# Kernel optimization log

Hardware: AMD Instinct MI355X
Metric: run time of the kernel (lower is better)

The kernel has to match this reference:

```python
import jax, jax.numpy as jnp
import numpy as np

B, S, D, V, H, L, NM = 16, 512, 768, 30522, 12, 12, 77
HD = D // H  # 64
FF = 4 * D
EPS = 1e-5


def setup_inputs() -> dict:
    key = jax.random.key(0)
    ks = jax.random.split(key, 32)
    sc = 0.02
    n = lambda k, shp: jax.random.normal(k, shp, dtype=jnp.float32) * sc
    d = {}
    d["token_ids"] = jax.random.randint(ks[0], (B, S), 0, V)
    d["segment_ids"] = jax.random.randint(ks[1], (B, S), 0, 2)
    d["mask_ids"] = jax.random.randint(ks[2], (B, NM), 0, S)
    d["tok_emb"] = n(ks[3], (V, D))
    d["pos_emb"] = n(ks[4], (S, D))
    d["seg_emb"] = n(ks[5], (2, D))
    d["dense_w"] = n(ks[6], (V, D))
    d["dense_b"] = jnp.zeros((V,), jnp.float32)
    # per-layer params stacked on leading L axis (torch Linear convention: y = x @ W.T + b)
    d["Wq"] = n(ks[7], (L, D, D)); d["bq"] = jnp.zeros((L, D), jnp.float32)
    d["Wk"] = n(ks[8], (L, D, D)); d["bk"] = jnp.zeros((L, D), jnp.float32)
    d["Wv"] = n(ks[9], (L, D, D)); d["bv"] = jnp.zeros((L, D), jnp.float32)
    d["Wo"] = n(ks[10], (L, D, D)); d["bo"] = jnp.zeros((L, D), jnp.float32)
    d["W1"] = n(ks[11], (L, FF, D)); d["b1"] = jnp.zeros((L, FF), jnp.float32)
    d["W2"] = n(ks[12], (L, D, FF)); d["b2"] = jnp.zeros((L, D), jnp.float32)
    d["g1"] = jnp.ones((L, D), jnp.float32); d["be1"] = jnp.zeros((L, D), jnp.float32)
    d["g2"] = jnp.ones((L, D), jnp.float32); d["be2"] = jnp.zeros((L, D), jnp.float32)
    return d


def _ln(x, g, b):
    m = jnp.mean(x, -1, keepdims=True)
    v = jnp.mean(jnp.square(x - m), -1, keepdims=True)
    return (x - m) * jax.lax.rsqrt(v + EPS) * g + b


def _encoder_stack(x, layer_params):
    def layer(x, p):
        Wq, bq, Wk, bk, Wv, bv, Wo, bo, W1, b1, W2, b2, g1, be1, g2, be2 = p
        q = (x @ Wq.T + bq).reshape(B, S, H, HD).transpose(0, 2, 1, 3)  # bhsd
        k = (x @ Wk.T + bk).reshape(B, S, H, HD).transpose(0, 2, 1, 3)
        v = (x @ Wv.T + bv).reshape(B, S, H, HD).transpose(0, 2, 1, 3)
        scores = jnp.einsum('bhqd,bhkd->bhqk', q, k) / jnp.sqrt(jnp.float32(HD))
        attn = jax.nn.softmax(scores, axis=-1)
        o = jnp.einsum('bhqk,bhkd->bhqd', attn, v).transpose(0, 2, 1, 3).reshape(B, S, D)
        x = _ln(x + (o @ Wo.T + bo), g1, be1)
        h = jax.nn.gelu(x @ W1.T + b1, approximate=False)  # torch nn.GELU default is exact
        h = h @ W2.T + b2
        return _ln(x + h, g2, be2), None
    x, _ = jax.lax.scan(layer, x, layer_params)
    return x


def reference(token_ids, segment_ids, mask_ids, tok_emb, pos_emb, seg_emb,
              dense_w, dense_b, Wq, bq, Wk, bk, Wv, bv, Wo, bo,
              W1, b1, W2, b2, g1, be1, g2, be2):
    x = tok_emb[token_ids] + seg_emb[segment_ids] + pos_emb[None, :, :]  # [B,S,D]
    x = _encoder_stack(x, (Wq, bq, Wk, bk, Wv, bv, Wo, bo, W1, b1, W2, b2, g1, be1, g2, be2))
    idx = jnp.broadcast_to(mask_ids[:, :, None], (B, NM, D))
    out = jnp.take_along_axis(x, idx, axis=1)  # [B,NM,D]
    return out @ dense_w.T + dense_b  # [B,NM,V]
```

## Files before the change

kernel.cpp:

```cpp
#include <hip/hip_runtime.h>
#include <stdint.h>

typedef uint16_t u16;
typedef uint32_t u32;
typedef uint64_t u64;
typedef short short8 __attribute__((ext_vector_type(8)));
typedef float f32x4 __attribute__((ext_vector_type(4)));

#define DEV static __device__ __forceinline__

DEV u16 f2bf(float f){
  u32 x = __builtin_bit_cast(u32, f);
  return (u16)((x + 0x7fffu + ((x >> 16) & 1u)) >> 16);
}

DEV float bf2f(u16 u){
  u32 v = (u32)u << 16;
  return __builtin_bit_cast(float, v);
}

DEV f32x4 mfma16(short8 a, short8 b, f32x4 c){
  return __builtin_amdgcn_mfma_f32_16x16x32_bf16(a, b, c, 0, 0, 0);
}

DEV void async16(const void* g, void* l){
  __builtin_amdgcn_global_load_lds(
      (const __attribute__((address_space(1))) u32*)g,
      (__attribute__((address_space(3))) u32*)l, 16, 0, 0);
}

__global__ __launch_bounds__(256)
void embed_kernel(const int* __restrict__ tid, const int* __restrict__ sid,
                  const float* __restrict__ tok, const float* __restrict__ pos,
                  const float* __restrict__ seg, u16* __restrict__ xb)
{
  const int row = blockIdx.x;
  const int s = row & 511;
  const int tk = tid[row], sg = sid[row];
  const int t = threadIdx.x;
#pragma unroll
  for (int e = 0; e < 3; ++e){
    int i = t + e*256;
    float v = tok[(u64)tk*768 + i] + seg[(u64)sg*768 + i] + pos[(u64)s*768 + i];
    xb[(u64)row*768 + i] = f2bf(v);
  }
}

__global__ __launch_bounds__(256)
void cvt_bf16(const float4* __restrict__ in, ushort4* __restrict__ out, int n4)
{
  int i = blockIdx.x*256 + threadIdx.x;
  if (i >= n4) return;
  float4 f = in[i];
  ushort4 o;
  o.x = f2bf(f.x); o.y = f2bf(f.y); o.z = f2bf(f.z); o.w = f2bf(f.w);
  out[i] = o;
}

__global__ __launch_bounds__(256)
void cvt_layer(const float4* __restrict__ Wq, const float4* __restrict__ Wk,
               const float4* __restrict__ Wv, const float4* __restrict__ Wo,
               const float4* __restrict__ W1, const float4* __restrict__ W2,
               ushort4* __restrict__ wqkv, ushort4* __restrict__ wob,
               ushort4* __restrict__ w1b, ushort4* __restrict__ w2b)
{
  const int i = blockIdx.x*256 + threadIdx.x;
  const int S = 147456;
  float4 f; ushort4* dst; int di;
  if      (i <   S)       { f = Wq[i];            dst = wqkv; di = i; }
  else if (i < 2*S)       { f = Wk[i - S];        dst = wqkv; di = i; }
  else if (i < 3*S)       { f = Wv[i - 2*S];      dst = wqkv; di = i; }
  else if (i < 4*S)       { f = Wo[i - 3*S];      dst = wob;  di = i - 3*S; }
  else if (i < 4*S+589824){ f = W1[i - 4*S];      dst = w1b;  di = i - 4*S; }
  else                    { f = W2[i - 4*S-589824]; dst = w2b; di = i - 4*S - 589824; }
  ushort4 o;
  o.x = f2bf(f.x); o.y = f2bf(f.y); o.z = f2bf(f.z); o.w = f2bf(f.w);
  dst[di] = o;
}

__global__ __launch_bounds__(256)
void concat_bias(const float* __restrict__ bq, const float* __restrict__ bk,
                 const float* __restrict__ bv, float* __restrict__ out)
{
  const int l = blockIdx.x;
  const int t = threadIdx.x;
#pragma unroll
  for (int e = 0; e < 3; ++e){
    int i = t + e*256;
    out[(u64)l*2304 + i]        = bq[(u64)l*768 + i];
    out[(u64)l*2304 + 768 + i]  = bk[(u64)l*768 + i];
    out[(u64)l*2304 + 1536 + i] = bv[(u64)l*768 + i];
  }
}

DEV void stage128(const u16* __restrict__ X, int ld, int limit,
                  int rowbase, int k0, u16* lds, int t)
{
  const int rl  = t >> 2;
  const int col = (((t & 3) ^ ((t >> 3) & 3))) << 3;
  int r0 = rowbase + rl;       if (r0 > limit-1) r0 = limit-1;
  int r1 = rowbase + rl + 64;  if (r1 > limit-1) r1 = limit-1;
  async16(X + (u64)r0*ld + k0 + col, lds + t*8);
  async16(X + (u64)r1*ld + k0 + col, lds + 2048 + t*8);
}

DEV short8 ldfrag(const u16* buf, int row, int slot){
  return *(const short8*)(buf + row*32 + (slot << 3));
}

template<int EPI>
__global__ __launch_bounds__(256)
void gemm3r(const u16* __restrict__ A, const u16* __restrict__ W,
            const float* __restrict__ bias, const u16* __restrict__ xres,
            u16* __restrict__ vt, void* __restrict__ Cout,
            int M, int N, int K, int GM)
{
  __shared__ u16 sm[24576];
  const int t = threadIdx.x;
  const int w = t >> 6, l = t & 63;
  const int lr = l & 15, lg = l >> 4;
  const int wm = (w >> 1)*64, wn = (w & 1)*64;
  const int xr = (lr >> 1) & 3;
  const int slot = lg ^ xr;

  const int nwg = gridDim.x, orig = blockIdx.x;
  const int q = nwg >> 3, r = nwg & 7;
  const int xcd = orig & 7, sl8 = orig >> 3;
  const int wgid = (xcd < r ? xcd*(q+1) : r*(q+1) + (xcd-r)*q) + sl8;
  const int bm = wgid % GM, bn = wgid / GM;

  f32x4 acc[4][4] = {};
  short8 af[4], bf[4];

  const int NT = K >> 5;
  stage128(A, K, M, bm*128,  0, sm,          t);
  stage128(W, K, N, bn*128,  0, sm + 4096,   t);
  stage128(A, K, M, bm*128, 32, sm + 8192,   t);
  stage128(W, K, N, bn*128, 32, sm + 12288,  t);
  asm volatile("s_waitcnt vmcnt(4)" ::: "memory");
  __builtin_amdgcn_s_barrier();

  for (int tt = 0; tt < NT; ++tt){
    const int rs  = (tt % 3) * 8192;
    const int rs2 = ((tt + 2) % 3) * 8192;
    const int k2  = (tt + 2) * 32;
    const bool st2 = (tt + 2) < NT;
    const u16* Ar = sm + rs;
    const u16* Br = sm + rs + 4096;

    af[0] = ldfrag(Ar, wm + lr, slot);
    af[1] = ldfrag(Ar, wm + 16 + lr, slot);
#pragma unroll
    for (int ni = 0; ni < 4; ++ni) bf[ni] = ldfrag(Br, wn + ni*16 + lr, slot);
    if (st2) stage128(A, K, M, bm*128, k2, sm + rs2, t);
    __builtin_amdgcn_s_barrier();
    __builtin_amdgcn_s_setprio(1);
#pragma unroll
    for (int mi = 0; mi < 2; ++mi)
#pragma unroll
      for (int ni = 0; ni < 4; ++ni)
        acc[mi][ni] = mfma16(af[mi], bf[ni], acc[mi][ni]);
    __builtin_amdgcn_s_setprio(0);
    __builtin_amdgcn_s_barrier();

    af[2] = ldfrag(Ar, wm + 32 + lr, slot);
    af[3] = ldfrag(Ar, wm + 48 + lr, slot);
    if (st2) stage128(W, K, N, bn*128, k2, sm + rs2 + 4096, t);
    __builtin_amdgcn_s_barrier();
    __builtin_amdgcn_s_setprio(1);
#pragma unroll
    for (int mi = 2; mi < 4; ++mi)
#pragma unroll
      for (int ni = 0; ni < 4; ++ni)
        acc[mi][ni] = mfma16(af[mi], bf[ni], acc[mi][ni]);
    __builtin_amdgcn_s_setprio(0);
    if (st2) asm volatile("s_waitcnt vmcnt(4)" ::: "memory");
    else     asm volatile("s_waitcnt vmcnt(0)" ::: "memory");
    __builtin_amdgcn_s_barrier();
  }

  __syncthreads();

  if constexpr (EPI == 1){
    if (vt && bn*128 + wn >= 1536){
      u16* vbuf = sm + w*4736;
#pragma unroll
      for (int mi = 0; mi < 4; ++mi)
#pragma unroll
        for (int ni = 0; ni < 4; ++ni){
          int col = bn*128 + wn + ni*16 + lr;
          float bv = bias ? bias[col] : 0.f;
#pragma unroll
          for (int rr = 0; rr < 4; ++rr)
            vbuf[(mi*16 + lg*4 + rr)*74 + ni*16 + lr] = f2bf(acc[mi][ni][rr] + bv);
        }
      asm volatile("s_waitcnt lgkmcnt(0)" ::: "memory");
      const int row0w = bm*128 + wm;
      const int b_ = row0w >> 9, s0 = row0w & 511;
      const int h_ = (bn*128 + wn - 1536) >> 6;
#pragma unroll
      for (int e = 0; e < 8; ++e){
        int d = e*8 + (l >> 3), s8 = (l & 7)*8;
        short8 ov;
#pragma unroll
        for (int i = 0; i < 8; ++i) ov[i] = (short)vbuf[(s8 + i)*74 + d];
        *(short8*)(vt + ((u64)(b_*12 + h_)*64 + d)*512 + s0 + s8) = ov;
      }
      return;
    }
  }

  constexpr int EPLD = 68;
  float* epw = (float*)sm + w*(16*EPLD);
#pragma unroll
  for (int mi = 0; mi < 4; ++mi){
#pragma unroll
    for (int ni = 0; ni < 4; ++ni){
      int col = bn*128 + wn + ni*16 + lr;
      float bv = bias ? bias[col < N ? col : N-1] : 0.f;
#pragma unroll
      for (int rr = 0; rr < 4; ++rr){
        float v = acc[mi][ni][rr] + bv;
        if constexpr (EPI == 2) v = 0.5f*v*(1.0f + erff(v*0.70710678118f));
        epw[(lg*4 + rr)*EPLD + ni*16 + lr] = v;
      }
    }
    asm volatile("s_waitcnt lgkmcnt(0)" ::: "memory");
    if constexpr (EPI == 0){
#pragma unroll
      for (int ps = 0; ps < 4; ++ps){
        int rloc = ps*4 + (l >> 4);
        int row = bm*128 + wm + mi*16 + rloc;
        int col = bn*128 + wn + (l & 15)*4;
        f32x4 v4 = *(const f32x4*)&epw[rloc*EPLD + (l & 15)*4];
        if (row < M){
          if (col + 3 < N){
            if (xres){
              ushort4 x4 = *(const ushort4*)(xres + (u64)row*N + col);
              v4[0] += bf2f(x4.x); v4[1] += bf2f(x4.y);
              v4[2] += bf2f(x4.z); v4[3] += bf2f(x4.w);
            }
            *(f32x4*)((float*)Cout + (u64)row*N + col) = v4;
          } else {
#pragma unroll
            for (int j = 0; j < 4; ++j)
              if (col + j < N){
                float vv = v4[j];
                if (xres) vv += bf2f(xres[(u64)row*N + col + j]);
                ((float*)Cout)[(u64)row*N + col + j] = vv;
              }
          }
        }
      }
    } else {
#pragma unroll
      for (int ps = 0; ps < 2; ++ps){
        int rloc = ps*8 + (l >> 3);
        int row = bm*128 + wm + mi*16 + rloc;
        int col = bn*128 + wn + (l & 7)*8;
        f32x4 a4 = *(const f32x4*)&epw[rloc*EPLD + (l & 7)*8];
        f32x4 b4 = *(const f32x4*)&epw[rloc*EPLD + (l & 7)*8 + 4];
        short8 o8;
        o8[0] = f2bf(a4[0]); o8[1] = f2bf(a4[1]); o8[2] = f2bf(a4[2]); o8[3] = f2bf(a4[3]);
        o8[4] = f2bf(b4[0]); o8[5] = f2bf(b4[1]); o8[6] = f2bf(b4[2]); o8[7] = f2bf(b4[3]);
        if (row < M){
          if (col + 7 < N) *(short8*)((u16*)Cout + (u64)row*N + col) = o8;
          else {
#pragma unroll
            for (int j = 0; j < 8; ++j)
              if (col + j < N) ((u16*)Cout)[(u64)row*N + col + j] = (u16)o8[j];
          }
        }
      }
    }
    asm volatile("s_waitcnt lgkmcnt(0)" ::: "memory");
  }
}

DEV void stage_tile(const u16* __restrict__ X, int ld, int limit,
                    int rowbase, int k0, u16* lds, int t)
{
  const int rl  = t >> 2;
  const int col = (((t & 3) ^ ((t >> 3) & 3))) << 3;
  int r0 = rowbase + rl;        if (r0 > limit-1) r0 = limit-1;
  int r1 = rowbase + rl + 128;  if (r1 > limit-1) r1 = limit-1;
  async16(X + (u64)r0*ld + k0 + col, lds + t*8);
  async16(X + (u64)r1*ld + k0 + col, lds + 4096 + t*8);
}

__global__ __launch_bounds__(512)
void gemm8v(const u16* __restrict__ A, const u16* __restrict__ W,
            const float* __restrict__ bias, float* __restrict__ Cout,
            int M, int N, int K, int GM)
{
  __shared__ u16 sm[49152];
  u16* Ab = sm;
  u16* Bb = sm + 24576;
  const int t = threadIdx.x;
  const int w = t >> 6, l = t & 63;
  const int lr = l & 15, lg = l >> 4;
  const int wr = w >> 2, wc = w & 3;
  const int xr = (lr >> 1) & 3;
  const int slot = lg ^ xr;

  const int nwg = gridDim.x, orig = blockIdx.x;
  const int q = nwg >> 3, r = nwg & 7;
  const int xcd = orig & 7, sl8 = orig >> 3;
  const int wgid = (xcd < r ? xcd*(q+1) : r*(q+1) + (xcd-r)*q) + sl8;
  const int bm = wgid % GM, bn = wgid / GM;

  f32x4 acc[8][4] = {};
  short8 afr[4], bfr[4];

  const int NT = K >> 5;
  stage_tile(A, K, M, bm*256,  0, Ab,        t);
  stage_tile(W, K, N, bn*256,  0, Bb,        t);
  stage_tile(A, K, M, bm*256, 32, Ab + 8192, t);
  stage_tile(W, K, N, bn*256, 32, Bb + 8192, t);
  asm volatile("s_waitcnt vmcnt(4)" ::: "memory");
  __builtin_amdgcn_s_barrier();

  for (int tt = 0; tt < NT; ++tt){
    const int rs = (tt % 3) * 8192;
    const int rs2 = ((tt + 2) % 3) * 8192;
    const int k2 = (tt + 2)*32;
    const u16* Ar = Ab + rs;
    const u16* Br = Bb + rs;
#pragma unroll
    for (int mi = 0; mi < 4; ++mi) afr[mi] = ldfrag(Ar, wr*128 + mi*16 + lr, slot);
#pragma unroll
    for (int ni = 0; ni < 4; ++ni) bfr[ni] = ldfrag(Br, wc*64 + ni*16 + lr, slot);
    if (tt + 2 < NT) stage_tile(A, K, M, bm*256, k2, Ab + rs2, t);
    __builtin_amdgcn_s_barrier();
    __builtin_amdgcn_s_setprio(1);
#pragma unroll
    for (int mi = 0; mi < 4; ++mi)
#pragma unroll
      for (int ni = 0; ni < 4; ++ni)
        acc[mi][ni] = mfma16(afr[mi], bfr[ni], acc[mi][ni]);
    __builtin_amdgcn_s_setprio(0);
    __builtin_amdgcn_s_barrier();
#pragma unroll
    for (int mi = 0; mi < 4; ++mi) afr[mi] = ldfrag(Ar, wr*128 + (mi+4)*16 + lr, slot);
    if (tt + 2 < NT) stage_tile(W, K, N, bn*256, k2, Bb + rs2, t);
    __builtin_amdgcn_s_barrier();
    __builtin_amdgcn_s_setprio(1);
#pragma unroll
    for (int mi = 0; mi < 4; ++mi)
#pragma unroll
      for (int ni = 0; ni < 4; ++ni)
        acc[mi+4][ni] = mfma16(afr[mi], bfr[ni], acc[mi+4][ni]);
    __builtin_amdgcn_s_setprio(0);
    if (tt + 2 < NT) asm volatile("s_waitcnt vmcnt(4)" ::: "memory");
    else             asm volatile("s_waitcnt vmcnt(0)" ::: "memory");
    __builtin_amdgcn_s_barrier();
  }

  __syncthreads();
  constexpr int EPLD = 68;
  float* epw = (float*)sm + w*(16*EPLD);
  const int growbase = bm*256 + wr*128;
  const int gcolbase = bn*256 + wc*64;
#pragma unroll
  for (int mi = 0; mi < 8; ++mi){
#pragma unroll
    for (int ni = 0; ni < 4; ++ni){
      int col = gcolbase + ni*16 + lr;
      float bv = bias ? bias[col < N ? col : N-1] : 0.f;
#pragma unroll
      for (int rr = 0; rr < 4; ++rr)
        epw[(lg*4 + rr)*EPLD + ni*16 + lr] = acc[mi][ni][rr] + bv;
    }
    asm volatile("s_waitcnt lgkmcnt(0)" ::: "memory");
#pragma unroll
    for (int ps = 0; ps < 4; ++ps){
      int rloc = ps*4 + (l >> 4);
      int row = growbase + mi*16 + rloc;
      int col = gcolbase + (l & 15)*4;
      f32x4 v4 = *(const f32x4*)&epw[rloc*EPLD + (l & 15)*4];
      if (row < M){
        if (col + 3 < N) *(f32x4*)(Cout + (u64)row*N + col) = v4;
        else {
#pragma unroll
          for (int j = 0; j < 4; ++j)
            if (col + j < N) Cout[(u64)row*N + col + j] = v4[j];
        }
      }
    }
    asm volatile("s_waitcnt lgkmcnt(0)" ::: "memory");
  }
}

__global__ __launch_bounds__(256)
void attn_kernel(const u16* __restrict__ qkv, const u16* __restrict__ vt,
                 u16* __restrict__ ob)
{
  __shared__ u16 p_lds[4][32][72];
  const int t = threadIdx.x, w = t >> 6, ll = t & 63;
  const int lr = ll & 15, lg = ll >> 4;
  const int qt = blockIdx.x, h = blockIdx.y, b = blockIdx.z;
  const int q0 = qt*128 + w*32;
  const float C = 0.125f * 1.44269504f;

  short8 qf[2][2];
#pragma unroll
  for (int f = 0; f < 2; ++f){
    const u16* qrow = qkv + (u64)(b*512 + q0 + f*16 + lr)*2304 + h*64 + 8*lg;
    qf[f][0] = *(const short8*)qrow;
    qf[f][1] = *(const short8*)(qrow + 32);
  }

  const u16* kbh = qkv + (u64)(b*512)*2304 + 768 + h*64;
  const u16* vth = vt + (u64)(b*12 + h)*64*512;

  f32x4 lacc[2] = {};
  f32x4 o_acc[2][4] = {};

  for (int jt = 0; jt < 8; ++jt){
    const int jb = jt*64;
    f32x4 s[2][4] = {};
#pragma unroll
    for (int jn = 0; jn < 4; ++jn){
      const u16* kr = kbh + (u64)(jb + jn*16 + lr)*2304 + 8*lg;
      short8 kf0 = *(const short8*)kr;
      short8 kf1 = *(const short8*)(kr + 32);
#pragma unroll
      for (int f = 0; f < 2; ++f){
        s[f][jn] = mfma16(qf[f][0], kf0, s[f][jn]);
        s[f][jn] = mfma16(qf[f][1], kf1, s[f][jn]);
      }
    }
#pragma unroll
    for (int f = 0; f < 2; ++f)
#pragma unroll
      for (int jn = 0; jn < 4; ++jn)
#pragma unroll
        for (int r = 0; r < 4; ++r){
          float pv = exp2f(s[f][jn][r]*C);
          lacc[f][r] += pv;
          p_lds[w][f*16 + 4*lg + r][jn*16 + lr] = f2bf(pv);
        }
    asm volatile("s_waitcnt lgkmcnt(0)" ::: "memory");
    short8 pa[2][2];
#pragma unroll
    for (int f = 0; f < 2; ++f){
      pa[f][0] = *(const short8*)(&p_lds[w][f*16 + lr][8*lg]);
      pa[f][1] = *(const short8*)(&p_lds[w][f*16 + lr][32 + 8*lg]);
    }
#pragma unroll
    for (int nd = 0; nd < 4; ++nd){
      const u16* vr = vth + (u64)(nd*16 + lr)*512 + jb + 8*lg;
      short8 vf0 = *(const short8*)vr;
      short8 vf1 = *(const short8*)(vr + 32);
#pragma unroll
      for (int f = 0; f < 2; ++f){
        o_acc[f][nd] = mfma16(pa[f][0], vf0, o_acc[f][nd]);
        o_acc[f][nd] = mfma16(pa[f][1], vf1, o_acc[f][nd]);
      }
    }
    asm volatile("s_waitcnt lgkmcnt(0)" ::: "memory");
  }
  float l_r[2][4];
#pragma unroll
  for (int f = 0; f < 2; ++f)
#pragma unroll
    for (int r = 0; r < 4; ++r){
      float v = lacc[f][r];
#pragma unroll
      for (int m = 1; m < 16; m <<= 1) v += __shfl_xor(v, m);
      l_r[f][r] = 1.f / v;
    }
#pragma unroll
  for (int f = 0; f < 2; ++f)
#pragma unroll
    for (int nd = 0; nd < 4; ++nd)
#pragma unroll
      for (int r = 0; r < 4; ++r)
        p_lds[w][f*16 + 4*lg + r][nd*16 + lr] = f2bf(o_acc[f][nd][r]*l_r[f][r]);
  asm volatile("s_waitcnt lgkmcnt(0)" ::: "memory");
#pragma unroll
  for (int ps = 0; ps < 4; ++ps){
    int row = ps*8 + (ll >> 3);
    short8 ov = *(const short8*)(&p_lds[w][row][(ll & 7)*8]);
    *(short8*)(ob + (u64)(b*512 + q0 + row)*768 + h*64 + (ll & 7)*8) = ov;
  }
}

__global__ __launch_bounds__(256)
void ln_only(const float* __restrict__ yin,
             const float* __restrict__ g, const float* __restrict__ be,
             u16* __restrict__ xbout)
{
  __shared__ float sred[8];
  const int row = blockIdx.x, t = threadIdx.x;
  const int w = t >> 6, ll = t & 63;
  float v[3]; float s = 0.f, sq = 0.f;
#pragma unroll
  for (int e = 0; e < 3; ++e){
    int i = t + e*256;
    float val = yin[(u64)row*768 + i];
    v[e] = val; s += val; sq += val*val;
  }
#pragma unroll
  for (int m = 1; m < 64; m <<= 1){ s += __shfl_xor(s, m); sq += __shfl_xor(sq, m); }
  if (ll == 0){ sred[w] = s; sred[4 + w] = sq; }
  __syncthreads();
  s  = sred[0] + sred[1] + sred[2] + sred[3];
  sq = sred[4] + sred[5] + sred[6] + sred[7];
  const float mean = s*(1.f/768.f);
  const float rstd = rsqrtf(sq*(1.f/768.f) - mean*mean + 1e-5f);
#pragma unroll
  for (int e = 0; e < 3; ++e){
    int i = t + e*256;
    xbout[(u64)row*768 + i] = f2bf((v[e] - mean)*rstd*g[i] + be[i]);
  }
}

__global__ __launch_bounds__(256)
void gather_rows(const u16* __restrict__ xb, const int* __restrict__ mids,
                 u16* __restrict__ xg)
{
  const int row = blockIdx.x;
  const int b = row / 77;
  const int src = b*512 + mids[row];
  const int t = threadIdx.x;
#pragma unroll
  for (int e = 0; e < 3; ++e){
    int i = t + e*256;
    xg[(u64)row*768 + i] = xb[(u64)src*768 + i];
  }
}

extern "C" void kernel_launch(void* const* d_in, const int* in_sizes, int n_in,
                              void* d_out, int out_size, void* d_ws, size_t ws_size,
                              hipStream_t stream)
{
  const int*   token_ids  = (const int*)  d_in[0];
  const int*   segment_ids= (const int*)  d_in[1];
  const int*   mask_ids   = (const int*)  d_in[2];
  const float* tok_emb    = (const float*)d_in[3];
  const float* pos_emb    = (const float*)d_in[4];
  const float* seg_emb    = (const float*)d_in[5];
  const float* dense_w    = (const float*)d_in[6];
  const float* dense_b    = (const float*)d_in[7];
  const float* Wq = (const float*)d_in[8];  const float* bq = (const float*)d_in[9];
  const float* Wk = (const float*)d_in[10]; const float* bk = (const float*)d_in[11];
  const float* Wv = (const float*)d_in[12]; const float* bv = (const float*)d_in[13];
  const float* Wo = (const float*)d_in[14]; const float* bo = (const float*)d_in[15];
  const float* W1 = (const float*)d_in[16]; const float* b1 = (const float*)d_in[17];
  const float* W2 = (const float*)d_in[18]; const float* b2 = (const float*)d_in[19];
  const float* g1 = (const float*)d_in[20]; const float* be1= (const float*)d_in[21];
  const float* g2 = (const float*)d_in[22]; const float* be2= (const float*)d_in[23];

  char* p = (char*)d_ws;
  auto alloc = [&](size_t bytes)->char*{
    char* r = p; p += (bytes + 255) & ~(size_t)255; return r;
  };
  const u64 T = 8192;
  float* y    = (float*)alloc(T*768*4);
  u16*   xb   = (u16*)  alloc(T*768*2);
  u16*   qkvb = (u16*)  alloc(T*2304*2);
  u16*   vT   = (u16*)  alloc(T*768*2);
  u16*   obuf = (u16*)  alloc(T*768*2);
  u16*   h1b  = (u16*)  alloc(T*3072*2);
  u16*   xg   = (u16*)  alloc((u64)1232*768*2);
  u16*   wqkv = (u16*)  alloc((u64)2304*768*2);
  u16*   wob  = (u16*)  alloc((u64)768*768*2);
  u16*   w1b  = (u16*)  alloc((u64)3072*768*2);
  u16*   w2b  = (u16*)  alloc((u64)3072*768*2);
  float* bqkv = (float*)alloc((u64)12*2304*4);
  u16*   dwb  = h1b;

  if ((size_t)(p - (char*)d_ws) > ws_size) return;

  embed_kernel<<<dim3(8192), dim3(256), 0, stream>>>(
      token_ids, segment_ids, tok_emb, pos_emb, seg_emb, xb);
  concat_bias<<<dim3(12), dim3(256), 0, stream>>>(bq, bk, bv, bqkv);

  for (int l = 0; l < 12; ++l){
    cvt_layer<<<dim3(6912), dim3(256), 0, stream>>>(
        (const float4*)(Wq + (u64)l*589824), (const float4*)(Wk + (u64)l*589824),
        (const float4*)(Wv + (u64)l*589824), (const float4*)(Wo + (u64)l*589824),
        (const float4*)(W1 + (u64)l*2359296), (const float4*)(W2 + (u64)l*2359296),
        (ushort4*)wqkv, (ushort4*)wob, (ushort4*)w1b, (ushort4*)w2b);

    gemm3r<1><<<dim3(64*18), dim3(256), 0, stream>>>(xb, wqkv, bqkv + (u64)l*2304, nullptr,
                                                     vT, qkvb, 8192, 2304, 768, 64);

    attn_kernel<<<dim3(4, 12, 16), dim3(256), 0, stream>>>(qkvb, vT, obuf);

    gemm3r<0><<<dim3(64*6), dim3(256), 0, stream>>>(obuf, wob, bo + (u64)l*768, xb,
                                                    nullptr, y, 8192, 768, 768, 64);
    ln_only<<<dim3(8192), dim3(256), 0, stream>>>(y, g1 + (u64)l*768, be1 + (u64)l*768, xb);

    gemm3r<2><<<dim3(64*24), dim3(256), 0, stream>>>(xb, w1b, b1 + (u64)l*3072, nullptr,
                                                     nullptr, h1b, 8192, 3072, 768, 64);
    gemm3r<0><<<dim3(64*6), dim3(256), 0, stream>>>(h1b, w2b, b2 + (u64)l*768, xb,
                                                    nullptr, y, 8192, 768, 3072, 64);
    ln_only<<<dim3(8192), dim3(256), 0, stream>>>(y, g2 + (u64)l*768, be2 + (u64)l*768, xb);
  }

  gather_rows<<<dim3(1232), dim3(256), 0, stream>>>(xb, mask_ids, xg);
  cvt_bf16<<<dim3(22892), dim3(256), 0, stream>>>((const float4*)dense_w, (ushort4*)dwb, 5860224);
  gemm8v<<<dim3(5*120), dim3(512), 0, stream>>>(xg, dwb, dense_b, (float*)d_out,
                                                1232, 30522, 768, 5);
}
```

Baseline: 3.673 ms.

## Fuse LayerNorm with next-layer weight conversion, wave-per-row LN, gather into final GEMM

LayerNorm now assigns one wavefront per row with vectorized loads and no LDS reduction. The second LN of each layer shares a launch with the bf16 conversion of the next layer's weights, so the per-layer cvt launch is gone and the two independent jobs run as one grid. The masked-row gather is folded into the vocab GEMM's A-tile loads, which removes the gather kernel and its buffer. The cost is a heterogeneous kernel with branch-divergent blocks, and the gather indexing assumes mask rows per batch equal 77 and a sequence length of 512.

```diff
diff --git a/kernel.cpp b/kernel.cpp
--- a/kernel.cpp
+++ b/kernel.cpp
@@ -57,14 +57,13 @@
   out[i] = o;
 }
 
-__global__ __launch_bounds__(256)
-void cvt_layer(const float4* __restrict__ Wq, const float4* __restrict__ Wk,
-               const float4* __restrict__ Wv, const float4* __restrict__ Wo,
-               const float4* __restrict__ W1, const float4* __restrict__ W2,
-               ushort4* __restrict__ wqkv, ushort4* __restrict__ wob,
-               ushort4* __restrict__ w1b, ushort4* __restrict__ w2b)
-{
-  const int i = blockIdx.x*256 + threadIdx.x;
+DEV void cvt_body(int i,
+                  const float4* __restrict__ Wq, const float4* __restrict__ Wk,
+                  const float4* __restrict__ Wv, const float4* __restrict__ Wo,
+                  const float4* __restrict__ W1, const float4* __restrict__ W2,
+                  ushort4* __restrict__ wqkv, ushort4* __restrict__ wob,
+                  ushort4* __restrict__ w1b, ushort4* __restrict__ w2b)
+{
   const int S = 147456;
   float4 f; ushort4* dst; int di;
   if      (i <   S)       { f = Wq[i];            dst = wqkv; di = i; }
@@ -79,6 +78,16 @@
 }
 
 __global__ __launch_bounds__(256)
+void cvt_layer(const float4* __restrict__ Wq, const float4* __restrict__ Wk,
+               const float4* __restrict__ Wv, const float4* __restrict__ Wo,
+               const float4* __restrict__ W1, const float4* __restrict__ W2,
+               ushort4* __restrict__ wqkv, ushort4* __restrict__ wob,
+               ushort4* __restrict__ w1b, ushort4* __restrict__ w2b)
+{
+  cvt_body(blockIdx.x*256 + threadIdx.x, Wq, Wk, Wv, Wo, W1, W2, wqkv, wob, w1b, w2b);
+}
+
+__global__ __launch_bounds__(256)
 void concat_bias(const float* __restrict__ bq, const float* __restrict__ bk,
                  const float* __restrict__ bv, float* __restrict__ out)
 {
@@ -90,6 +99,61 @@
     out[(u64)l*2304 + i]        = bq[(u64)l*768 + i];
     out[(u64)l*2304 + 768 + i]  = bk[(u64)l*768 + i];
     out[(u64)l*2304 + 1536 + i] = bv[(u64)l*768 + i];
+  }
+}
+
+DEV void ln_row(const float* __restrict__ yr, const float* __restrict__ g,
+                const float* __restrict__ be, u16* __restrict__ xr, int ll)
+{
+  f32x4 v[3]; float s = 0.f, sq = 0.f;
+#pragma unroll
+  for (int e = 0; e < 3; ++e){
+    v[e] = *(const f32x4*)(yr + e*256 + ll*4);
+#pragma unroll
+    for (int j = 0; j < 4; ++j){ s += v[e][j]; sq += v[e][j]*v[e][j]; }
+  }
+#pragma unroll
+  for (int m = 1; m < 64; m <<= 1){ s += __shfl_xor(s, m); sq += __shfl_xor(sq, m); }
+  const float mean = s*(1.f/768.f);
+  const float rstd = rsqrtf(sq*(1.f/768.f) - mean*mean + 1e-5f);
+#pragma unroll
+  for (int e = 0; e < 3; ++e){
+    f32x4 gv = *(const f32x4*)(g  + e*256 + ll*4);
+    f32x4 bv = *(const f32x4*)(be + e*256 + ll*4);
+    ushort4 o;
+    o.x = f2bf((v[e][0] - mean)*rstd*gv[0] + bv[0]);
+    o.y = f2bf((v[e][1] - mean)*rstd*gv[1] + bv[1]);
+    o.z = f2bf((v[e][2] - mean)*rstd*gv[2] + bv[2]);
+    o.w = f2bf((v[e][3] - mean)*rstd*gv[3] + bv[3]);
+    *(ushort4*)(xr + e*256 + ll*4) = o;
+  }
+}
+
+__global__ __launch_bounds__(256)
+void ln_wave(const float* __restrict__ yin, const float* __restrict__ g,
+             const float* __restrict__ be, u16* __restrict__ xbout)
+{
+  const int t = threadIdx.x, w = t >> 6, ll = t & 63;
+  const u64 row = (u64)blockIdx.x*4 + w;
+  ln_row(yin + row*768, g, be, xbout + row*768, ll);
+}
+
+__global__ __launch_bounds__(256)
+void ln2cvt(const float* __restrict__ yin, const float* __restrict__ g,
+            const float* __restrict__ be, u16* __restrict__ xbout,
+            const float4* __restrict__ Wq, const float4* __restrict__ Wk,
+            const float4* __restrict__ Wv, const float4* __restrict__ Wo,
+            const float4* __restrict__ W1, const float4* __restrict__ W2,
+            ushort4* __restrict__ wqkv, ushort4* __restrict__ wob,
+            ushort4* __restrict__ w1b, ushort4* __restrict__ w2b)
+{
+  if (blockIdx.x < 2048){
+    const int t = threadIdx.x, w = t >> 6, ll = t & 63;
+    const u64 row = (u64)blockIdx.x*4 + w;
+    ln_row(yin + row*768, g, be, xbout + row*768, ll);
+  } else {
+    cvt_body((blockIdx.x - 2048)*256 + threadIdx.x,
+             Wq, Wk, Wv, Wo, W1, W2, wqkv, wob, w1b, w2b);
   }
 }
 
@@ -289,7 +353,8 @@
 }
 
 __global__ __launch_bounds__(512)
-void gemm8v(const u16* __restrict__ A, const u16* __restrict__ W,
+void gemm8v(const u16* __restrict__ xb, const int* __restrict__ mids,
+            const u16* __restrict__ W,
             const float* __restrict__ bias, float* __restrict__ Cout,
             int M, int N, int K, int GM)
 {
@@ -309,13 +374,22 @@
   const int wgid = (xcd < r ? xcd*(q+1) : r*(q+1) + (xcd-r)*q) + sl8;
   const int bm = wgid % GM, bn = wgid / GM;
 
+  const int rl_ = t >> 2;
+  const int colsw = (((t & 3) ^ ((t >> 3) & 3))) << 3;
+  int r0 = bm*256 + rl_;        if (r0 > M-1) r0 = M-1;
+  int r1 = bm*256 + rl_ + 128;  if (r1 > M-1) r1 = M-1;
+  const int g0 = (r0/77)*512 + mids[r0];
+  const int g1 = (r1/77)*512 + mids[r1];
+  const u16* pa0 = xb + (u64)g0*768 + colsw;
+  const u16* pa1 = xb + (u64)g1*768 + colsw;
+
   f32x4 acc[8][4] = {};
   short8 afr[4], bfr[4];
 
   const int NT = K >> 5;
-  stage_tile(A, K, M, bm*256,  0, Ab,        t);
+  async16(pa0, Ab + t*8); async16(pa1, Ab + 4096 + t*8);
   stage_tile(W, K, N, bn*256,  0, Bb,        t);
-  stage_tile(A, K, M, bm*256, 32, Ab + 8192, t);
+  async16(pa0 + 32, Ab + 8192 + t*8); async16(pa1 + 32, Ab + 12288 + t*8);
   stage_tile(W, K, N, bn*256, 32, Bb + 8192, t);
   asm volatile("s_waitcnt vmcnt(4)" ::: "memory");
   __builtin_amdgcn_s_barrier();
@@ -330,7 +404,10 @@
     for (int mi = 0; mi < 4; ++mi) afr[mi] = ldfrag(Ar, wr*128 + mi*16 + lr, slot);
 #pragma unroll
     for (int ni = 0; ni < 4; ++ni) bfr[ni] = ldfrag(Br, wc*64 + ni*16 + lr, slot);
-    if (tt + 2 < NT) stage_tile(A, K, M, bm*256, k2, Ab + rs2, t);
+    if (tt + 2 < NT){
+      async16(pa0 + k2, Ab + rs2 + t*8);
+      async16(pa1 + k2, Ab + rs2 + 4096 + t*8);
+    }
     __builtin_amdgcn_s_barrier();
     __builtin_amdgcn_s_setprio(1);
 #pragma unroll
@@ -483,51 +560,6 @@
     int row = ps*8 + (ll >> 3);
     short8 ov = *(const short8*)(&p_lds[w][row][(ll & 7)*8]);
     *(short8*)(ob + (u64)(b*512 + q0 + row)*768 + h*64 + (ll & 7)*8) = ov;
-  }
-}
-
-__global__ __launch_bounds__(256)
-void ln_only(const float* __restrict__ yin,
-             const float* __restrict__ g, const float* __restrict__ be,
-             u16* __restrict__ xbout)
-{
-  __shared__ float sred[8];
-  const int row = blockIdx.x, t = threadIdx.x;
-  const int w = t >> 6, ll = t & 63;
-  float v[3]; float s = 0.f, sq = 0.f;
-#pragma unroll
-  for (int e = 0; e < 3; ++e){
-    int i = t + e*256;
-    float val = yin[(u64)row*768 + i];
-    v[e] = val; s += val; sq += val*val;
-  }
-#pragma unroll
-  for (int m = 1; m < 64; m <<= 1){ s += __shfl_xor(s, m); sq += __shfl_xor(sq, m); }
-  if (ll == 0){ sred[w] = s; sred[4 + w] = sq; }
-  __syncthreads();
-  s  = sred[0] + sred[1] + sred[2] + sred[3];
-  sq = sred[4] + sred[5] + sred[6] + sred[7];
-  const float mean = s*(1.f/768.f);
-  const float rstd = rsqrtf(sq*(1.f/768.f) - mean*mean + 1e-5f);
-#pragma unroll
-  for (int e = 0; e < 3; ++e){
-    int i = t + e*256;
-    xbout[(u64)row*768 + i] = f2bf((v[e] - mean)*rstd*g[i] + be[i]);
-  }
-}
-
-__global__ __launch_bounds__(256)
-void gather_rows(const u16* __restrict__ xb, const int* __restrict__ mids,
-                 u16* __restrict__ xg)
-{
-  const int row = blockIdx.x;
-  const int b = row / 77;
-  const int src = b*512 + mids[row];
-  const int t = threadIdx.x;
-#pragma unroll
-  for (int e = 0; e < 3; ++e){
-    int i = t + e*256;
-    xg[(u64)row*768 + i] = xb[(u64)src*768 + i];
   }
 }
 
@@ -563,7 +595,6 @@
   u16*   vT   = (u16*)  alloc(T*768*2);
   u16*   obuf = (u16*)  alloc(T*768*2);
   u16*   h1b  = (u16*)  alloc(T*3072*2);
-  u16*   xg   = (u16*)  alloc((u64)1232*768*2);
   u16*   wqkv = (u16*)  alloc((u64)2304*768*2);
   u16*   wob  = (u16*)  alloc((u64)768*768*2);
   u16*   w1b  = (u16*)  alloc((u64)3072*768*2);
@@ -576,14 +607,12 @@
   embed_kernel<<<dim3(8192), dim3(256), 0, stream>>>(
       token_ids, segment_ids, tok_emb, pos_emb, seg_emb, xb);
   concat_bias<<<dim3(12), dim3(256), 0, stream>>>(bq, bk, bv, bqkv);
+  cvt_layer<<<dim3(6912), dim3(256), 0, stream>>>(
+      (const float4*)Wq, (const float4*)Wk, (const float4*)Wv, (const float4*)Wo,
+      (const float4*)W1, (const float4*)W2,
+      (ushort4*)wqkv, (ushort4*)wob, (ushort4*)w1b, (ushort4*)w2b);
 
   for (int l = 0; l < 12; ++l){
-    cvt_layer<<<dim3(6912), dim3(256), 0, stream>>>(
-        (const float4*)(Wq + (u64)l*589824), (const float4*)(Wk + (u64)l*589824),
-        (const float4*)(Wv + (u64)l*589824), (const float4*)(Wo + (u64)l*589824),
-        (const float4*)(W1 + (u64)l*2359296), (const float4*)(W2 + (u64)l*2359296),
-        (ushort4*)wqkv, (ushort4*)wob, (ushort4*)w1b, (ushort4*)w2b);
-
     gemm3r<1><<<dim3(64*18), dim3(256), 0, stream>>>(xb, wqkv, bqkv + (u64)l*2304, nullptr,
                                                      vT, qkvb, 8192, 2304, 768, 64);
 
@@ -591,17 +620,25 @@
 
     gemm3r<0><<<dim3(64*6), dim3(256), 0, stream>>>(obuf, wob, bo + (u64)l*768, xb,
                                                     nullptr, y, 8192, 768, 768, 64);
-    ln_only<<<dim3(8192), dim3(256), 0, stream>>>(y, g1 + (u64)l*768, be1 + (u64)l*768, xb);
+    ln_wave<<<dim3(2048), dim3(256), 0, stream>>>(y, g1 + (u64)l*768, be1 + (u64)l*768, xb);
 
     gemm3r<2><<<dim3(64*24), dim3(256), 0, stream>>>(xb, w1b, b1 + (u64)l*3072, nullptr,
                                                      nullptr, h1b, 8192, 3072, 768, 64);
     gemm3r<0><<<dim3(64*6), dim3(256), 0, stream>>>(h1b, w2b, b2 + (u64)l*768, xb,
                                                     nullptr, y, 8192, 768, 3072, 64);
-    ln_only<<<dim3(8192), dim3(256), 0, stream>>>(y, g2 + (u64)l*768, be2 + (u64)l*768, xb);
-  }
-
-  gather_rows<<<dim3(1232), dim3(256), 0, stream>>>(xb, mask_ids, xg);
+    if (l < 11){
+      ln2cvt<<<dim3(2048 + 6912), dim3(256), 0, stream>>>(
+          y, g2 + (u64)l*768, be2 + (u64)l*768, xb,
+          (const float4*)(Wq + (u64)(l+1)*589824), (const float4*)(Wk + (u64)(l+1)*589824),
+          (const float4*)(Wv + (u64)(l+1)*589824), (const float4*)(Wo + (u64)(l+1)*589824),
+          (const float4*)(W1 + (u64)(l+1)*2359296), (const float4*)(W2 + (u64)(l+1)*2359296),
+          (ushort4*)wqkv, (ushort4*)wob, (ushort4*)w1b, (ushort4*)w2b);
+    } else {
+      ln_wave<<<dim3(2048), dim3(256), 0, stream>>>(y, g2 + (u64)l*768, be2 + (u64)l*768, xb);
+    }
+  }
+
   cvt_bf16<<<dim3(22892), dim3(256), 0, stream>>>((const float4*)dense_w, (ushort4*)dwb, 5860224);
-  gemm8v<<<dim3(5*120), dim3(512), 0, stream>>>(xg, dwb, dense_b, (float*)d_out,
+  gemm8v<<<dim3(5*120), dim3(512), 0, stream>>>(xb, mask_ids, dwb, dense_b, (float*)d_out,
                                                 1232, 30522, 768, 5);
 }
```

Measured after the change: 3.609 ms. Within noise of the previous version (-1.7%).
